# Kernel tuning notes

Hardware: AMD Instinct MI355X
Metric: run time of the kernel (lower is better)

The kernel has to match this reference:

```python
import jax, jax.numpy as jnp
import numpy as np

B, S, D, H = 2, 2048, 1024, 16
DK = D // H


def setup_inputs() -> dict:
    key = jax.random.key(0)
    ks = jax.random.split(key, 12)
    scale = 1.0 / np.sqrt(D)
    inp = {
        "Q": jax.random.normal(ks[0], (B, S, D), jnp.float32),
        "K": jax.random.normal(ks[1], (B, S, D), jnp.float32),
        "V": jax.random.normal(ks[2], (B, S, D), jnp.float32),
        # causal mask, broadcast over batch: [B, S, S]
        "mask": jnp.broadcast_to(jnp.tril(jnp.ones((S, S), jnp.bool_)), (B, S, S)),
        "WQ_w": jax.random.normal(ks[3], (D, D), jnp.float32) * scale,
        "WQ_b": jnp.zeros((D,), jnp.float32),
        "WK_w": jax.random.normal(ks[4], (D, D), jnp.float32) * scale,
        "WK_b": jnp.zeros((D,), jnp.float32),
        "WV_w": jax.random.normal(ks[5], (D, D), jnp.float32) * scale,
        "WV_b": jnp.zeros((D,), jnp.float32),
        "WO_w": jax.random.normal(ks[6], (D, D), jnp.float32) * scale,
        "WO_b": jnp.zeros((D,), jnp.float32),
    }
    return inp


def reference(Q, K, V, mask, WQ_w, WQ_b, WK_w, WK_b, WV_w, WV_b, WO_w, WO_b):
    # Linear projections (torch Linear: x @ W.T + b), split heads -> [B,H,S,DK]
    def proj(x, w, b):
        return (x @ w.T + b).reshape(B, S, H, DK).transpose(0, 2, 1, 3)

    q = proj(Q, WQ_w, WQ_b)
    k = proj(K, WK_w, WK_b)
    v = proj(V, WV_w, WV_b)

    scores = jnp.einsum("bhqd,bhkd->bhqk", q, k) / jnp.sqrt(jnp.asarray(DK, q.dtype))
    scores = jnp.where(mask[:, None, :, :], scores, -jnp.inf)
    attn = jax.nn.softmax(scores, axis=-1)  # dropout is identity in eval mode

    out = jnp.einsum("bhqk,bhkd->bhqd", attn, v)
    out = out.transpose(0, 2, 1, 3).reshape(B, S, D)
    out = out @ WO_w.T + WO_b
    return (out, attn)
```

## Files before the change

### kernel.cpp

```cpp
#include <hip/hip_runtime.h>

#define S_LEN 2048
#define DMODEL 1024
#define NHEAD 16
#define DKH 64
#define BATCH 2

typedef __bf16 bf16_t;
typedef __bf16 bf16x8 __attribute__((ext_vector_type(8)));
typedef __bf16 bf16x4 __attribute__((ext_vector_type(4)));
typedef float f32x4 __attribute__((ext_vector_type(4)));

__device__ __forceinline__ void gload16(const bf16_t* g, bf16_t* l) {
  __builtin_amdgcn_global_load_lds(
      (const __attribute__((address_space(1))) unsigned int*)g,
      (__attribute__((address_space(3))) unsigned int*)l,
      16, 0, 0);
}

__global__ void cvt_all(const float* __restrict__ Q, const float* __restrict__ K,
                        const float* __restrict__ V, const float* __restrict__ WQ,
                        const float* __restrict__ WK, const float* __restrict__ WV,
                        const float* __restrict__ WO, bf16_t* __restrict__ dst) {
  const int i = blockIdx.x * 256 + threadIdx.x;
  const float* src;
  int off;
  if (i < 1572864) {
    const int seg = i >> 19;
    off = i & 524287;
    src = (seg == 0) ? Q : ((seg == 1) ? K : V);
  } else {
    const int j = i - 1572864;
    const int seg = j >> 17;
    off = j & 131071;
    src = (seg == 0) ? WQ : ((seg == 1) ? WK : ((seg == 2) ? WV : WO));
  }
  f32x4 a = *(const f32x4*)(src + (size_t)off * 8);
  f32x4 b = *(const f32x4*)(src + (size_t)off * 8 + 4);
  bf16x8 v;
#pragma unroll
  for (int j = 0; j < 4; ++j) { v[j] = (bf16_t)a[j]; v[4 + j] = (bf16_t)b[j]; }
  *(bf16x8*)(dst + (size_t)i * 8) = v;
}

struct GOp {
  const bf16_t* A;
  const bf16_t* W;
  const float* bias;
  char* out;
  int emode;
};

#define GM 4096
#define GN 1024
#define GK 1024
#define BM 128
#define BN 128
#define BK 64

__launch_bounds__(256, 2)
__global__ void gemm_bf16(GOp op0, GOp op1, GOp op2) {
  GOp op = (blockIdx.z == 0) ? op0 : ((blockIdx.z == 1) ? op1 : op2);
  const int n0 = blockIdx.x * BN;
  const int m0 = blockIdx.y * BM;
  const int t = threadIdx.x;
  const int w = t >> 6;
  const int l = t & 63;
  const int wr = w >> 1, wc = w & 1;
  const int lg = l >> 4, ll = l & 15;

  __shared__ __align__(16) bf16_t Asm[BM * BK];
  __shared__ __align__(16) bf16_t Bsm[BN * BK];

  f32x4 acc[4][4] = {};

  const int sr = l >> 3;
  const int sc = l & 7;

  for (int kt = 0; kt < GK / BK; ++kt) {
    __syncthreads();
#pragma unroll
    for (int i = 0; i < 4; ++i) {
      const int rbase = i * 32 + (w << 3);
      const int row = rbase + sr;
      const int gc = (sc ^ (row & 7)) << 3;
      gload16(op.A + (size_t)(m0 + row) * GK + kt * BK + gc, &Asm[rbase * BK]);
      gload16(op.W + (size_t)(n0 + row) * GK + kt * BK + gc, &Bsm[rbase * BK]);
    }
    __syncthreads();

    bf16x8 af[4][2], bfr[4][2];
#pragma unroll
    for (int mi = 0; mi < 4; ++mi) {
      const int row = wr * 64 + mi * 16 + ll;
      af[mi][0] = *(const bf16x8*)&Asm[row * BK + ((lg ^ (row & 7)) << 3)];
      af[mi][1] = *(const bf16x8*)&Asm[row * BK + (((4 + lg) ^ (row & 7)) << 3)];
    }
#pragma unroll
    for (int ni = 0; ni < 4; ++ni) {
      const int row = wc * 64 + ni * 16 + ll;
      bfr[ni][0] = *(const bf16x8*)&Bsm[row * BK + ((lg ^ (row & 7)) << 3)];
      bfr[ni][1] = *(const bf16x8*)&Bsm[row * BK + (((4 + lg) ^ (row & 7)) << 3)];
    }
#pragma unroll
    for (int mi = 0; mi < 4; ++mi)
#pragma unroll
      for (int ni = 0; ni < 4; ++ni) {
        acc[mi][ni] = __builtin_amdgcn_mfma_f32_16x16x32_bf16(af[mi][0], bfr[ni][0], acc[mi][ni], 0, 0, 0);
        acc[mi][ni] = __builtin_amdgcn_mfma_f32_16x16x32_bf16(af[mi][1], bfr[ni][1], acc[mi][ni], 0, 0, 0);
      }
  }

#pragma unroll
  for (int mi = 0; mi < 4; ++mi) {
#pragma unroll
    for (int ni = 0; ni < 4; ++ni) {
      const int col = n0 + wc * 64 + ni * 16 + ll;
      const int rbase = m0 + wr * 64 + mi * 16 + (lg << 2);
      const float bval = op.bias[col];
      f32x4 v = acc[mi][ni];
      if (op.emode == 0) {
        bf16_t* o = (bf16_t*)op.out;
#pragma unroll
        for (int r = 0; r < 4; ++r)
          o[(size_t)(rbase + r) * GN + col] = (bf16_t)(v[r] + bval);
      } else if (op.emode == 1) {
        const int hh = col >> 6, dd = col & 63;
        const int bb = rbase >> 11, ss = rbase & (S_LEN - 1);
        bf16_t* o = (bf16_t*)op.out + (((size_t)bb * NHEAD + hh) * DKH + dd) * S_LEN + ss;
        bf16x4 pk;
#pragma unroll
        for (int r = 0; r < 4; ++r) pk[r] = (bf16_t)(v[r] + bval);
        *(bf16x4*)o = pk;
      } else {
        float* o = (float*)op.out;
#pragma unroll
        for (int r = 0; r < 4; ++r)
          o[(size_t)(rbase + r) * GN + col] = v[r] + bval;
      }
    }
  }
}

__launch_bounds__(256, 2)
__global__ void attn2(const bf16_t* __restrict__ qp, const bf16_t* __restrict__ kp,
                      const bf16_t* __restrict__ vT, float* __restrict__ attn_out,
                      bf16_t* __restrict__ ctx) {
  const int raw = blockIdx.x;
  const int wg = (raw & 7) * 64 + (raw >> 3);
  const int bh = wg >> 4;
  const int pr = wg & 15;
  const int b = bh >> 4, h = bh & 15;
  const int flip = wg & 1;

  __shared__ __align__(16) bf16_t Qs[64 * 64];
  __shared__ __align__(16) bf16_t Ks[64 * 64];
  __shared__ __align__(16) bf16_t Vs[64 * 64];
  __shared__ __align__(16) bf16_t Pt[4][16 * 64];

  const int t = threadIdx.x;
  const int w = t >> 6;
  const int l = t & 63;
  const int lg = l >> 4;
  const int ll = l & 15;
  const int sr = l >> 3;
  const int sc = l & 7;

  for (int half = 0; half < 2; ++half) {
    const int qt = (half ^ flip) ? (31 - pr) : pr;
    const int q0 = qt * 64;
    const int nkt = qt + 1;

    __syncthreads();
#pragma unroll
    for (int i = 0; i < 2; ++i) {
      const int rbase = i * 32 + (w << 3);
      const int row = rbase + sr;
      const int gc = (sc ^ (row & 7)) << 3;
      gload16(qp + (size_t)(b * S_LEN + q0 + row) * DMODEL + h * DKH + gc, &Qs[rbase * 64]);
    }
    __syncthreads();

    bf16x8 qf0, qf1;
    {
      const int row = w * 16 + ll;
      qf0 = *(const bf16x8*)&Qs[row * 64 + ((lg ^ (row & 7)) << 3)];
      qf1 = *(const bf16x8*)&Qs[row * 64 + (((4 + lg) ^ (row & 7)) << 3)];
    }

    f32x4 oacc[4] = {};
    float sums[4] = {0.f, 0.f, 0.f, 0.f};
    const int qrow_base = q0 + w * 16 + (lg << 2);

    for (int kt = 0; kt < nkt; ++kt) {
      __syncthreads();
#pragma unroll
      for (int i = 0; i < 2; ++i) {
        const int rbase = i * 32 + (w << 3);
        const int row = rbase + sr;
        const int gc = (sc ^ (row & 7)) << 3;
        gload16(kp + (size_t)(b * S_LEN + kt * 64 + row) * DMODEL + h * DKH + gc, &Ks[rbase * 64]);
        gload16(vT + ((size_t)bh * DKH + row) * S_LEN + kt * 64 + gc, &Vs[rbase * 64]);
      }
      __syncthreads();

      const bool diag = (kt == qt);
#pragma unroll
      for (int cb = 0; cb < 4; ++cb) {
        const int krow = cb * 16 + ll;
        bf16x8 kf0 = *(const bf16x8*)&Ks[krow * 64 + ((lg ^ (krow & 7)) << 3)];
        bf16x8 kf1 = *(const bf16x8*)&Ks[krow * 64 + (((4 + lg) ^ (krow & 7)) << 3)];
        f32x4 a = {0.f, 0.f, 0.f, 0.f};
        a = __builtin_amdgcn_mfma_f32_16x16x32_bf16(qf0, kf0, a, 0, 0, 0);
        a = __builtin_amdgcn_mfma_f32_16x16x32_bf16(qf1, kf1, a, 0, 0, 0);
        const int gcol = kt * 64 + krow;
        if (diag) {
#pragma unroll
          for (int r = 0; r < 4; ++r) {
            const float e = (gcol <= qrow_base + r) ? __expf(a[r] * 0.125f) : 0.0f;
            sums[r] += e;
            const int ql = (lg << 2) + r;
            const int k = cb * 16 + ll;
            *(bf16_t*)((char*)&Pt[w][0] + ql * 128 + (((k >> 3) ^ (ql & 7)) << 4) + ((k & 7) << 1)) = (bf16_t)e;
          }
        } else {
#pragma unroll
          for (int r = 0; r < 4; ++r) {
            const float e = __expf(a[r] * 0.125f);
            sums[r] += e;
            const int ql = (lg << 2) + r;
            const int k = cb * 16 + ll;
            *(bf16_t*)((char*)&Pt[w][0] + ql * 128 + (((k >> 3) ^ (ql & 7)) << 4) + ((k & 7) << 1)) = (bf16_t)e;
          }
        }
      }
      bf16x8 pa0 = *(const bf16x8*)((char*)&Pt[w][0] + ll * 128 + ((lg ^ (ll & 7)) << 4));
      bf16x8 pa1 = *(const bf16x8*)((char*)&Pt[w][0] + ll * 128 + (((4 + lg) ^ (ll & 7)) << 4));
#pragma unroll
      for (int db = 0; db < 4; ++db) {
        const int drow = db * 16 + ll;
        bf16x8 vf0 = *(const bf16x8*)&Vs[drow * 64 + ((lg ^ (drow & 7)) << 3)];
        bf16x8 vf1 = *(const bf16x8*)&Vs[drow * 64 + (((4 + lg) ^ (drow & 7)) << 3)];
        oacc[db] = __builtin_amdgcn_mfma_f32_16x16x32_bf16(pa0, vf0, oacc[db], 0, 0, 0);
        oacc[db] = __builtin_amdgcn_mfma_f32_16x16x32_bf16(pa1, vf1, oacc[db], 0, 0, 0);
      }
    }

    float rinv[4];
#pragma unroll
    for (int r = 0; r < 4; ++r) {
      float s = sums[r];
      s += __shfl_xor(s, 1);
      s += __shfl_xor(s, 2);
      s += __shfl_xor(s, 4);
      s += __shfl_xor(s, 8);
      rinv[r] = 1.0f / s;
    }

#pragma unroll
    for (int db = 0; db < 4; ++db)
#pragma unroll
      for (int r = 0; r < 4; ++r) {
        const int grow = q0 + w * 16 + (lg << 2) + r;
        ctx[(size_t)(b * S_LEN + grow) * DMODEL + h * DKH + db * 16 + ll] = (bf16_t)(oacc[db][r] * rinv[r]);
      }

    float* arow = attn_out + ((size_t)bh * S_LEN + q0) * S_LEN;
    for (int kt = 0; kt <= qt; ++kt) {
      __syncthreads();
#pragma unroll
      for (int i = 0; i < 2; ++i) {
        const int rbase = i * 32 + (w << 3);
        const int row = rbase + sr;
        const int gc = (sc ^ (row & 7)) << 3;
        gload16(kp + (size_t)(b * S_LEN + kt * 64 + row) * DMODEL + h * DKH + gc, &Ks[rbase * 64]);
      }
      __syncthreads();

      const bool diag = (kt == qt);
#pragma unroll
      for (int cb = 0; cb < 4; ++cb) {
        const int krow = cb * 16 + ll;
        bf16x8 kf0 = *(const bf16x8*)&Ks[krow * 64 + ((lg ^ (krow & 7)) << 3)];
        bf16x8 kf1 = *(const bf16x8*)&Ks[krow * 64 + (((4 + lg) ^ (krow & 7)) << 3)];
        f32x4 a = {0.f, 0.f, 0.f, 0.f};
        a = __builtin_amdgcn_mfma_f32_16x16x32_bf16(qf0, kf0, a, 0, 0, 0);
        a = __builtin_amdgcn_mfma_f32_16x16x32_bf16(qf1, kf1, a, 0, 0, 0);
        const int gcol = kt * 64 + krow;
        if (diag) {
#pragma unroll
          for (int r = 0; r < 4; ++r) {
            const float e = (gcol <= qrow_base + r) ? __expf(a[r] * 0.125f) * rinv[r] : 0.0f;
            arow[(size_t)(w * 16 + (lg << 2) + r) * S_LEN + gcol] = e;
          }
        } else {
#pragma unroll
          for (int r = 0; r < 4; ++r)
            arow[(size_t)(w * 16 + (lg << 2) + r) * S_LEN + gcol] = __expf(a[r] * 0.125f) * rinv[r];
        }
      }
    }
    for (int kt = qt + 1; kt < 32; ++kt) {
      f32x4 z = {0.f, 0.f, 0.f, 0.f};
#pragma unroll
      for (int j = 0; j < 4; ++j) {
        const int row = w * 16 + (lg << 2) + j;
        *(f32x4*)(arow + (size_t)row * S_LEN + kt * 64 + (ll << 2)) = z;
      }
    }
  }
}

extern "C" void kernel_launch(void* const* d_in, const int* in_sizes, int n_in,
                              void* d_out, int out_size, void* d_ws, size_t ws_size,
                              hipStream_t stream) {
  const float* Q   = (const float*)d_in[0];
  const float* K   = (const float*)d_in[1];
  const float* V   = (const float*)d_in[2];
  const float* WQw = (const float*)d_in[4];
  const float* WQb = (const float*)d_in[5];
  const float* WKw = (const float*)d_in[6];
  const float* WKb = (const float*)d_in[7];
  const float* WVw = (const float*)d_in[8];
  const float* WVb = (const float*)d_in[9];
  const float* WOw = (const float*)d_in[10];
  const float* WOb = (const float*)d_in[11];

  char* ws = (char*)d_ws;
  bf16_t* qb  = (bf16_t*)(ws);
  bf16_t* kb  = (bf16_t*)(ws + (size_t)( 8 << 20));
  bf16_t* vb  = (bf16_t*)(ws + (size_t)(16 << 20));
  bf16_t* wq  = (bf16_t*)(ws + (size_t)(24 << 20));
  bf16_t* wk  = (bf16_t*)(ws + (size_t)(26 << 20));
  bf16_t* wv  = (bf16_t*)(ws + (size_t)(28 << 20));
  bf16_t* wo  = (bf16_t*)(ws + (size_t)(30 << 20));
  bf16_t* qp  = (bf16_t*)(ws + (size_t)(32 << 20));
  bf16_t* kp  = (bf16_t*)(ws + (size_t)(40 << 20));
  bf16_t* vT  = (bf16_t*)(ws + (size_t)(48 << 20));
  bf16_t* ctx = (bf16_t*)(ws + (size_t)(56 << 20));

  float* out_main = (float*)d_out;
  float* attn_out = out_main + (size_t)BATCH * S_LEN * DMODEL;

  cvt_all<<<dim3(8192), 256, 0, stream>>>(Q, K, V, WQw, WKw, WVw, WOw, (bf16_t*)ws);

  GOp opq{qb, wq, WQb, (char*)qp, 0};
  GOp opk{kb, wk, WKb, (char*)kp, 0};
  GOp opv{vb, wv, WVb, (char*)vT, 1};
  gemm_bf16<<<dim3(8, 32, 3), 256, 0, stream>>>(opq, opk, opv);

  attn2<<<dim3(512), 256, 0, stream>>>(qp, kp, vT, attn_out, ctx);

  GOp opo{ctx, wo, WOb, (char*)out_main, 2};
  gemm_bf16<<<dim3(8, 32, 1), 256, 0, stream>>>(opo, opo, opo);
}
```

Baseline: 224.5 us.

## Restructure attention into double-buffered, interleaved two-tile pipeline with fused passes

The attention kernel now double-buffers K/V tiles in shared memory so the next tile's load is issued before computing the current one. It also interleaves the second (probability-writing) pass of the long query tile with the first (accumulation) pass of the short tile, so each K tile load serves both. Masked zero tiles are written inside these loops, and attention probabilities go out through nontemporal vector stores. The score MFMA is transposed so each lane owns one query row and writes a 16-byte chunk, and the GEMM launch bounds are raised to 3 blocks per CU. This adds register pressure and shared memory use, which may limit occupancy.

```diff
diff --git a/kernel.cpp b/kernel.cpp
--- a/kernel.cpp
+++ b/kernel.cpp
@@ -58,7 +58,7 @@
 #define BN 128
 #define BK 64
 
-__launch_bounds__(256, 2)
+__launch_bounds__(256, 3)
 __global__ void gemm_bf16(GOp op0, GOp op1, GOp op2) {
   GOp op = (blockIdx.z == 0) ? op0 : ((blockIdx.z == 1) ? op1 : op2);
   const int n0 = blockIdx.x * BN;
@@ -68,14 +68,13 @@
   const int l = t & 63;
   const int wr = w >> 1, wc = w & 1;
   const int lg = l >> 4, ll = l & 15;
-
-  __shared__ __align__(16) bf16_t Asm[BM * BK];
-  __shared__ __align__(16) bf16_t Bsm[BN * BK];
-
-  f32x4 acc[4][4] = {};
-
   const int sr = l >> 3;
   const int sc = l & 7;
+
+  __shared__ __align__(16) bf16_t Asm[BM * BK];
+  __shared__ __align__(16) bf16_t Bsm[BM * BK];
+
+  f32x4 acc[4][4] = {};
 
   for (int kt = 0; kt < GK / BK; ++kt) {
     __syncthreads();
@@ -143,7 +142,7 @@
 }
 
 __launch_bounds__(256, 2)
-__global__ void attn2(const bf16_t* __restrict__ qp, const bf16_t* __restrict__ kp,
+__global__ void attn3(const bf16_t* __restrict__ qp, const bf16_t* __restrict__ kp,
                       const bf16_t* __restrict__ vT, float* __restrict__ attn_out,
                       bf16_t* __restrict__ ctx) {
   const int raw = blockIdx.x;
@@ -151,12 +150,15 @@
   const int bh = wg >> 4;
   const int pr = wg & 15;
   const int b = bh >> 4, h = bh & 15;
-  const int flip = wg & 1;
+  const int qa = pr;
+  const int qb = 31 - pr;
+  const int a0 = qa * 64, b0 = qb * 64;
 
   __shared__ __align__(16) bf16_t Qs[64 * 64];
-  __shared__ __align__(16) bf16_t Ks[64 * 64];
-  __shared__ __align__(16) bf16_t Vs[64 * 64];
+  __shared__ __align__(16) bf16_t Ks[2][64 * 64];
+  __shared__ __align__(16) bf16_t Vs[2][64 * 64];
   __shared__ __align__(16) bf16_t Pt[4][16 * 64];
+  float* rinvS = (float*)&Pt[0][0];
 
   const int t = threadIdx.x;
   const int w = t >> 6;
@@ -166,149 +168,221 @@
   const int sr = l >> 3;
   const int sc = l & 7;
 
-  for (int half = 0; half < 2; ++half) {
-    const int qt = (half ^ flip) ? (31 - pr) : pr;
-    const int q0 = qt * 64;
-    const int nkt = qt + 1;
-
+  const bf16_t* kbh = kp + (size_t)b * S_LEN * DMODEL + h * DKH;
+  const bf16_t* vbh = vT + (size_t)bh * DKH * S_LEN;
+  float* aoutA = attn_out + ((size_t)bh * S_LEN + a0) * S_LEN;
+  float* aoutB = attn_out + ((size_t)bh * S_LEN + b0) * S_LEN;
+  const f32x4 zero4 = {0.f, 0.f, 0.f, 0.f};
+
+#define KV_STAGE(bu, kt_)                                                             \
+  {                                                                                   \
+    _Pragma("unroll") for (int i = 0; i < 2; ++i) {                                   \
+      const int rbase = i * 32 + (w << 3);                                            \
+      const int row = rbase + sr;                                                     \
+      const int gc = (sc ^ (row & 7)) << 3;                                           \
+      gload16(kbh + (size_t)((kt_) * 64 + row) * DMODEL + gc, &Ks[bu][rbase * 64]);   \
+      gload16(vbh + (size_t)row * S_LEN + (kt_) * 64 + gc, &Vs[bu][rbase * 64]);      \
+    }                                                                                 \
+  }
+
+#define K_STAGE(bu, kt_)                                                              \
+  {                                                                                   \
+    _Pragma("unroll") for (int i = 0; i < 2; ++i) {                                   \
+      const int rbase = i * 32 + (w << 3);                                            \
+      const int row = rbase + sr;                                                     \
+      const int gc = (sc ^ (row & 7)) << 3;                                           \
+      gload16(kbh + (size_t)((kt_) * 64 + row) * DMODEL + gc, &Ks[bu][rbase * 64]);   \
+    }                                                                                 \
+  }
+
+#define Q_STAGE(q0_)                                                                  \
+  {                                                                                   \
+    _Pragma("unroll") for (int i = 0; i < 2; ++i) {                                   \
+      const int rbase = i * 32 + (w << 3);                                            \
+      const int row = rbase + sr;                                                     \
+      const int gc = (sc ^ (row & 7)) << 3;                                           \
+      gload16(qp + (size_t)(b * S_LEN + (q0_) + row) * DMODEL + h * DKH + gc, &Qs[rbase * 64]); \
+    }                                                                                 \
+  }
+
+#define Q_FRAGS(qf0_, qf1_)                                                           \
+  {                                                                                   \
+    const int row = w * 16 + ll;                                                      \
+    qf0_ = *(const bf16x8*)&Qs[row * 64 + ((lg ^ (row & 7)) << 3)];                   \
+    qf1_ = *(const bf16x8*)&Qs[row * 64 + (((4 + lg) ^ (row & 7)) << 3)];             \
+  }
+
+#define L1_BODY(qf0_, qf1_, q0_, kt_, cur_, ssum_, oacc_, diag_)                      \
+  {                                                                                   \
+    _Pragma("unroll") for (int i = 0; i < 4; ++i) {                                   \
+      const int lr = i * 16 + ll;                                                     \
+      bf16x8 kf0 = *(const bf16x8*)&Ks[cur_][lr * 64 + ((lg ^ (lr & 7)) << 3)];       \
+      bf16x8 kf1 = *(const bf16x8*)&Ks[cur_][lr * 64 + (((4 + lg) ^ (lr & 7)) << 3)]; \
+      f32x4 s_ = {0.f, 0.f, 0.f, 0.f};                                                \
+      s_ = __builtin_amdgcn_mfma_f32_16x16x32_bf16(kf0, qf0_, s_, 0, 0, 0);           \
+      s_ = __builtin_amdgcn_mfma_f32_16x16x32_bf16(kf1, qf1_, s_, 0, 0, 0);           \
+      const int kb_ = (kt_) * 64 + i * 16 + (lg << 2);                                \
+      bf16x4 pk_;                                                                     \
+      if (diag_) {                                                                    \
+        const int qrow_ = (q0_) + w * 16 + ll;                                        \
+        _Pragma("unroll") for (int r = 0; r < 4; ++r) {                               \
+          const float e_ = (kb_ + r <= qrow_) ? __expf(s_[r] * 0.125f) : 0.0f;        \
+          ssum_ += e_;                                                                \
+          pk_[r] = (bf16_t)e_;                                                        \
+        }                                                                             \
+      } else {                                                                        \
+        _Pragma("unroll") for (int r = 0; r < 4; ++r) {                               \
+          const float e_ = __expf(s_[r] * 0.125f);                                    \
+          ssum_ += e_;                                                                \
+          pk_[r] = (bf16_t)e_;                                                        \
+        }                                                                             \
+      }                                                                               \
+      const int c_ = i * 2 + (lg >> 1);                                               \
+      *(bf16x4*)((char*)&Pt[w][0] + ll * 128 + ((c_ ^ (ll & 7)) << 4) + ((lg & 1) << 3)) = pk_; \
+    }                                                                                 \
+    bf16x8 pa0 = *(const bf16x8*)((char*)&Pt[w][0] + ll * 128 + ((lg ^ (ll & 7)) << 4));       \
+    bf16x8 pa1 = *(const bf16x8*)((char*)&Pt[w][0] + ll * 128 + (((4 + lg) ^ (ll & 7)) << 4)); \
+    _Pragma("unroll") for (int db = 0; db < 4; ++db) {                                \
+      const int drow = db * 16 + ll;                                                  \
+      bf16x8 vf0 = *(const bf16x8*)&Vs[cur_][drow * 64 + ((lg ^ (drow & 7)) << 3)];   \
+      bf16x8 vf1 = *(const bf16x8*)&Vs[cur_][drow * 64 + (((4 + lg) ^ (drow & 7)) << 3)]; \
+      oacc_[db] = __builtin_amdgcn_mfma_f32_16x16x32_bf16(pa0, vf0, oacc_[db], 0, 0, 0); \
+      oacc_[db] = __builtin_amdgcn_mfma_f32_16x16x32_bf16(pa1, vf1, oacc_[db], 0, 0, 0); \
+    }                                                                                 \
+  }
+
+#define L2_BODY(qf0_, qf1_, q0_, kt_, cur_, rv_, arow_, diag_)                        \
+  {                                                                                   \
+    _Pragma("unroll") for (int i = 0; i < 4; ++i) {                                   \
+      const int lr = i * 16 + ll;                                                     \
+      bf16x8 kf0 = *(const bf16x8*)&Ks[cur_][lr * 64 + ((lg ^ (lr & 7)) << 3)];       \
+      bf16x8 kf1 = *(const bf16x8*)&Ks[cur_][lr * 64 + (((4 + lg) ^ (lr & 7)) << 3)]; \
+      f32x4 s_ = {0.f, 0.f, 0.f, 0.f};                                                \
+      s_ = __builtin_amdgcn_mfma_f32_16x16x32_bf16(kf0, qf0_, s_, 0, 0, 0);           \
+      s_ = __builtin_amdgcn_mfma_f32_16x16x32_bf16(kf1, qf1_, s_, 0, 0, 0);           \
+      const int kb_ = (kt_) * 64 + i * 16 + (lg << 2);                                \
+      f32x4 o_;                                                                       \
+      if (diag_) {                                                                    \
+        const int qrow_ = (q0_) + w * 16 + ll;                                        \
+        _Pragma("unroll") for (int r = 0; r < 4; ++r)                                 \
+          o_[r] = (kb_ + r <= qrow_) ? __expf(s_[r] * 0.125f) * (rv_) : 0.0f;         \
+      } else {                                                                        \
+        _Pragma("unroll") for (int r = 0; r < 4; ++r)                                 \
+          o_[r] = __expf(s_[r] * 0.125f) * (rv_);                                     \
+      }                                                                               \
+      __builtin_nontemporal_store(o_, (f32x4*)((arow_) + (size_t)(w * 16 + ll) * S_LEN + kb_)); \
+    }                                                                                 \
+  }
+
+#define ZERO_TILE(base_, ktz_)                                                        \
+  {                                                                                   \
+    _Pragma("unroll") for (int jj = 0; jj < 4; ++jj)                                  \
+      __builtin_nontemporal_store(zero4,                                              \
+          (f32x4*)((base_) + (size_t)(w * 16 + (jj << 2) + lg) * S_LEN + (ktz_) * 64 + (ll << 2))); \
+  }
+
+  Q_STAGE(b0);
+  KV_STAGE(0, 0);
+  __syncthreads();
+  bf16x8 qfb0, qfb1;
+  Q_FRAGS(qfb0, qfb1);
+
+  f32x4 oaccB[4] = {};
+  float ssumB = 0.f;
+  int cur = 0;
+
+  for (int kt = 0; kt <= qb; ++kt) {
+    if (kt < qb) KV_STAGE(cur ^ 1, kt + 1);
+    if (kt < qb) ZERO_TILE(aoutA, qa + 1 + kt);
+    __builtin_amdgcn_s_setprio(1);
+    L1_BODY(qfb0, qfb1, b0, kt, cur, ssumB, oaccB, (kt == qb));
+    __builtin_amdgcn_s_setprio(0);
     __syncthreads();
-#pragma unroll
-    for (int i = 0; i < 2; ++i) {
-      const int rbase = i * 32 + (w << 3);
-      const int row = rbase + sr;
-      const int gc = (sc ^ (row & 7)) << 3;
-      gload16(qp + (size_t)(b * S_LEN + q0 + row) * DMODEL + h * DKH + gc, &Qs[rbase * 64]);
+    cur ^= 1;
+  }
+
+  {
+    float s = ssumB;
+    s += __shfl_xor(s, 16);
+    s += __shfl_xor(s, 32);
+    if (lg == 0) rinvS[w * 16 + ll] = 1.0f / s;
+  }
+  Q_STAGE(a0);
+  KV_STAGE(0, 0);
+  __syncthreads();
+
+  {
+    float rv4[4];
+#pragma unroll
+    for (int r = 0; r < 4; ++r) rv4[r] = rinvS[w * 16 + (lg << 2) + r];
+#pragma unroll
+    for (int db = 0; db < 4; ++db)
+#pragma unroll
+      for (int r = 0; r < 4; ++r) {
+        const int grow = b0 + w * 16 + (lg << 2) + r;
+        ctx[(size_t)(b * S_LEN + grow) * DMODEL + h * DKH + db * 16 + ll] = (bf16_t)(oaccB[db][r] * rv4[r]);
+      }
+  }
+  const float rvb = rinvS[w * 16 + ll];
+  bf16x8 qfa0, qfa1;
+  Q_FRAGS(qfa0, qfa1);
+
+  f32x4 oaccA[4] = {};
+  float ssumA = 0.f;
+  cur = 0;
+
+  for (int kt = 0; kt <= qb; ++kt) {
+    if (kt < qb) {
+      if (kt + 1 <= qa) KV_STAGE(cur ^ 1, kt + 1) else K_STAGE(cur ^ 1, kt + 1);
+    }
+    if (kt < qa) ZERO_TILE(aoutB, qb + 1 + kt);
+    L2_BODY(qfb0, qfb1, b0, kt, cur, rvb, aoutB, (kt == qb));
+    if (kt <= qa) {
+      __builtin_amdgcn_s_setprio(1);
+      L1_BODY(qfa0, qfa1, a0, kt, cur, ssumA, oaccA, (kt == qa));
+      __builtin_amdgcn_s_setprio(0);
     }
     __syncthreads();
-
-    bf16x8 qf0, qf1;
-    {
-      const int row = w * 16 + ll;
-      qf0 = *(const bf16x8*)&Qs[row * 64 + ((lg ^ (row & 7)) << 3)];
-      qf1 = *(const bf16x8*)&Qs[row * 64 + (((4 + lg) ^ (row & 7)) << 3)];
-    }
-
-    f32x4 oacc[4] = {};
-    float sums[4] = {0.f, 0.f, 0.f, 0.f};
-    const int qrow_base = q0 + w * 16 + (lg << 2);
-
-    for (int kt = 0; kt < nkt; ++kt) {
-      __syncthreads();
-#pragma unroll
-      for (int i = 0; i < 2; ++i) {
-        const int rbase = i * 32 + (w << 3);
-        const int row = rbase + sr;
-        const int gc = (sc ^ (row & 7)) << 3;
-        gload16(kp + (size_t)(b * S_LEN + kt * 64 + row) * DMODEL + h * DKH + gc, &Ks[rbase * 64]);
-        gload16(vT + ((size_t)bh * DKH + row) * S_LEN + kt * 64 + gc, &Vs[rbase * 64]);
+    cur ^= 1;
+  }
+
+  {
+    float s = ssumA;
+    s += __shfl_xor(s, 16);
+    s += __shfl_xor(s, 32);
+    if (lg == 0) rinvS[w * 16 + ll] = 1.0f / s;
+  }
+  K_STAGE(0, 0);
+  __syncthreads();
+
+  {
+    float rv4[4];
+#pragma unroll
+    for (int r = 0; r < 4; ++r) rv4[r] = rinvS[w * 16 + (lg << 2) + r];
+#pragma unroll
+    for (int db = 0; db < 4; ++db)
+#pragma unroll
+      for (int r = 0; r < 4; ++r) {
+        const int grow = a0 + w * 16 + (lg << 2) + r;
+        ctx[(size_t)(b * S_LEN + grow) * DMODEL + h * DKH + db * 16 + ll] = (bf16_t)(oaccA[db][r] * rv4[r]);
       }
-      __syncthreads();
-
-      const bool diag = (kt == qt);
-#pragma unroll
-      for (int cb = 0; cb < 4; ++cb) {
-        const int krow = cb * 16 + ll;
-        bf16x8 kf0 = *(const bf16x8*)&Ks[krow * 64 + ((lg ^ (krow & 7)) << 3)];
-        bf16x8 kf1 = *(const bf16x8*)&Ks[krow * 64 + (((4 + lg) ^ (krow & 7)) << 3)];
-        f32x4 a = {0.f, 0.f, 0.f, 0.f};
-        a = __builtin_amdgcn_mfma_f32_16x16x32_bf16(qf0, kf0, a, 0, 0, 0);
-        a = __builtin_amdgcn_mfma_f32_16x16x32_bf16(qf1, kf1, a, 0, 0, 0);
-        const int gcol = kt * 64 + krow;
-        if (diag) {
-#pragma unroll
-          for (int r = 0; r < 4; ++r) {
-            const float e = (gcol <= qrow_base + r) ? __expf(a[r] * 0.125f) : 0.0f;
-            sums[r] += e;
-            const int ql = (lg << 2) + r;
-            const int k = cb * 16 + ll;
-            *(bf16_t*)((char*)&Pt[w][0] + ql * 128 + (((k >> 3) ^ (ql & 7)) << 4) + ((k & 7) << 1)) = (bf16_t)e;
-          }
-        } else {
-#pragma unroll
-          for (int r = 0; r < 4; ++r) {
-            const float e = __expf(a[r] * 0.125f);
-            sums[r] += e;
-            const int ql = (lg << 2) + r;
-            const int k = cb * 16 + ll;
-            *(bf16_t*)((char*)&Pt[w][0] + ql * 128 + (((k >> 3) ^ (ql & 7)) << 4) + ((k & 7) << 1)) = (bf16_t)e;
-          }
-        }
-      }
-      bf16x8 pa0 = *(const bf16x8*)((char*)&Pt[w][0] + ll * 128 + ((lg ^ (ll & 7)) << 4));
-      bf16x8 pa1 = *(const bf16x8*)((char*)&Pt[w][0] + ll * 128 + (((4 + lg) ^ (ll & 7)) << 4));
-#pragma unroll
-      for (int db = 0; db < 4; ++db) {
-        const int drow = db * 16 + ll;
-        bf16x8 vf0 = *(const bf16x8*)&Vs[drow * 64 + ((lg ^ (drow & 7)) << 3)];
-        bf16x8 vf1 = *(const bf16x8*)&Vs[drow * 64 + (((4 + lg) ^ (drow & 7)) << 3)];
-        oacc[db] = __builtin_amdgcn_mfma_f32_16x16x32_bf16(pa0, vf0, oacc[db], 0, 0, 0);
-        oacc[db] = __builtin_amdgcn_mfma_f32_16x16x32_bf16(pa1, vf1, oacc[db], 0, 0, 0);
-      }
-    }
-
-    float rinv[4];
-#pragma unroll
-    for (int r = 0; r < 4; ++r) {
-      float s = sums[r];
-      s += __shfl_xor(s, 1);
-      s += __shfl_xor(s, 2);
-      s += __shfl_xor(s, 4);
-      s += __shfl_xor(s, 8);
-      rinv[r] = 1.0f / s;
-    }
-
-#pragma unroll
-    for (int db = 0; db < 4; ++db)
-#pragma unroll
-      for (int r = 0; r < 4; ++r) {
-        const int grow = q0 + w * 16 + (lg << 2) + r;
-        ctx[(size_t)(b * S_LEN + grow) * DMODEL + h * DKH + db * 16 + ll] = (bf16_t)(oacc[db][r] * rinv[r]);
-      }
-
-    float* arow = attn_out + ((size_t)bh * S_LEN + q0) * S_LEN;
-    for (int kt = 0; kt <= qt; ++kt) {
-      __syncthreads();
-#pragma unroll
-      for (int i = 0; i < 2; ++i) {
-        const int rbase = i * 32 + (w << 3);
-        const int row = rbase + sr;
-        const int gc = (sc ^ (row & 7)) << 3;
-        gload16(kp + (size_t)(b * S_LEN + kt * 64 + row) * DMODEL + h * DKH + gc, &Ks[rbase * 64]);
-      }
-      __syncthreads();
-
-      const bool diag = (kt == qt);
-#pragma unroll
-      for (int cb = 0; cb < 4; ++cb) {
-        const int krow = cb * 16 + ll;
-        bf16x8 kf0 = *(const bf16x8*)&Ks[krow * 64 + ((lg ^ (krow & 7)) << 3)];
-        bf16x8 kf1 = *(const bf16x8*)&Ks[krow * 64 + (((4 + lg) ^ (krow & 7)) << 3)];
-        f32x4 a = {0.f, 0.f, 0.f, 0.f};
-        a = __builtin_amdgcn_mfma_f32_16x16x32_bf16(qf0, kf0, a, 0, 0, 0);
-        a = __builtin_amdgcn_mfma_f32_16x16x32_bf16(qf1, kf1, a, 0, 0, 0);
-        const int gcol = kt * 64 + krow;
-        if (diag) {
-#pragma unroll
-          for (int r = 0; r < 4; ++r) {
-            const float e = (gcol <= qrow_base + r) ? __expf(a[r] * 0.125f) * rinv[r] : 0.0f;
-            arow[(size_t)(w * 16 + (lg << 2) + r) * S_LEN + gcol] = e;
-          }
-        } else {
-#pragma unroll
-          for (int r = 0; r < 4; ++r)
-            arow[(size_t)(w * 16 + (lg << 2) + r) * S_LEN + gcol] = __expf(a[r] * 0.125f) * rinv[r];
-        }
-      }
-    }
-    for (int kt = qt + 1; kt < 32; ++kt) {
-      f32x4 z = {0.f, 0.f, 0.f, 0.f};
-#pragma unroll
-      for (int j = 0; j < 4; ++j) {
-        const int row = w * 16 + (lg << 2) + j;
-        *(f32x4*)(arow + (size_t)row * S_LEN + kt * 64 + (ll << 2)) = z;
-      }
-    }
-  }
+  }
+  const float rva = rinvS[w * 16 + ll];
+  cur = 0;
+
+  for (int kt = 0; kt <= qa; ++kt) {
+    if (kt < qa) K_STAGE(cur ^ 1, kt + 1);
+    L2_BODY(qfa0, qfa1, a0, kt, cur, rva, aoutA, (kt == qa));
+    __syncthreads();
+    cur ^= 1;
+  }
+#undef KV_STAGE
+#undef K_STAGE
+#undef Q_STAGE
+#undef Q_FRAGS
+#undef L1_BODY
+#undef L2_BODY
+#undef ZERO_TILE
 }
 
 extern "C" void kernel_launch(void* const* d_in, const int* in_sizes, int n_in,
@@ -349,7 +423,7 @@
   GOp opv{vb, wv, WVb, (char*)vT, 1};
   gemm_bf16<<<dim3(8, 32, 3), 256, 0, stream>>>(opq, opk, opv);
 
-  attn2<<<dim3(512), 256, 0, stream>>>(qp, kp, vT, attn_out, ctx);
+  attn3<<<dim3(512), 256, 0, stream>>>(qp, kp, vT, attn_out, ctx);
 
   GOp opo{ctx, wo, WOb, (char*)out_main, 2};
   gemm_bf16<<<dim3(8, 32, 1), 256, 0, stream>>>(opo, opo, opo);
```

Result: slower. 273.1 us (+21.6%).
